# Performance work log

Hardware: AMD Instinct MI355X
Metric: run time of the kernel (lower is better)

Reference implementation:

```python
import math
import jax, jax.numpy as jnp
import numpy as np

NQ, NK = 16384, 4096
QDIM, KDIM, MID = 512, 256, 256


def setup_inputs() -> dict:
    key = jax.random.key(0)
    k1, k2, k3, k4, k5, k6, k7, k8 = jax.random.split(key, 8)
    return {
        "global_embeddings": jax.random.normal(k1, (NQ, QDIM), dtype=jnp.float32),
        "substruct_embeddings": jax.random.normal(k2, (NK, KDIM), dtype=jnp.float32),
        "substruct_weight": jax.random.uniform(k3, (NK,), dtype=jnp.float32),
        "mask": jax.random.randint(k4, (NQ, NK), 0, 2, dtype=jnp.int32),
        "Wq": jax.random.normal(k5, (MID, QDIM), dtype=jnp.float32) / math.sqrt(QDIM),
        "bq": jax.random.normal(k6, (MID,), dtype=jnp.float32) * 0.01,
        "Wk": jax.random.normal(k7, (MID, KDIM), dtype=jnp.float32) / math.sqrt(KDIM),
        "bk": jax.random.normal(k8, (MID,), dtype=jnp.float32) * 0.01,
    }


def reference(global_embeddings, substruct_embeddings, substruct_weight, mask, Wq, bq, Wk, bk):
    # Q/K projections (torch Linear: x @ W.T + b)
    Q = global_embeddings @ Wq.T + bq            # [NQ, MID]
    K = substruct_embeddings @ Wk.T + bk         # [NK, MID]
    scores = (Q @ K.T) / math.sqrt(MID)          # [NQ, NK]
    scores = jnp.where(mask == 0, -jnp.inf, scores)
    attn = jax.nn.softmax(scores, axis=-1)       # row-wise stable softmax
    # torch.diag(w) @ E  ==  elementwise row scaling
    V = substruct_weight[:, None] * substruct_embeddings  # [NK, KDIM]
    return attn @ V                              # [NQ, KDIM]
```

## Files before the change

kernel.cpp:

```cpp
#include <hip/hip_runtime.h>
#include <hip/hip_bf16.h>

typedef __bf16 bf16_t;
typedef bf16_t bf16x8 __attribute__((ext_vector_type(8)));
typedef float  f32x4  __attribute__((ext_vector_type(4)));
typedef unsigned long long u64;
typedef unsigned int u32;

#define MFMA16(A,B,C) __builtin_amdgcn_mfma_f32_16x16x32_bf16((A),(B),(C),0,0,0)


static __device__ __forceinline__ void gl_lds16(const bf16_t* g, void* l) {
    __builtin_amdgcn_global_load_lds(
        (const __attribute__((address_space(1))) u32*)(const void*)g,
        (__attribute__((address_space(3))) u32*)l, 16, 0, 0);
}

template<int KA, bool SWZ>
__global__ __launch_bounds__(256)
void proj_kernel(const float* __restrict__ A, const float* __restrict__ W,
                 const float* __restrict__ b, bf16_t* __restrict__ C,
                 float scale)
{
    __shared__ bf16_t Alds[64][40];
    __shared__ bf16_t Wlds[256][40];

    const int t  = threadIdx.x;
    const int w  = t >> 6, l = t & 63, lr = l & 15, lg = l >> 4;
    const int m0 = blockIdx.x * 64;

    f32x4 acc[16];
#pragma unroll
    for (int tt = 0; tt < 16; ++tt) acc[tt] = (f32x4){0.f, 0.f, 0.f, 0.f};

    const int ar  = t >> 2;
    const int ac8 = (t & 3) * 8;

    for (int kb = 0; kb < KA / 32; ++kb) {
        {
            const float* ap = A + (size_t)(m0 + ar) * KA + kb * 32 + ac8;
            float4 a0 = *(const float4*)ap;
            float4 a1 = *(const float4*)(ap + 4);
            bf16x8 av;
            av[0]=(bf16_t)a0.x; av[1]=(bf16_t)a0.y; av[2]=(bf16_t)a0.z; av[3]=(bf16_t)a0.w;
            av[4]=(bf16_t)a1.x; av[5]=(bf16_t)a1.y; av[6]=(bf16_t)a1.z; av[7]=(bf16_t)a1.w;
            *(bf16x8*)&Alds[ar][ac8] = av;
        }
#pragma unroll
        for (int c = 0; c < 4; ++c) {
            int e8 = c * 256 + t;
            int wr = e8 >> 2, wc8 = (e8 & 3) * 8;
            const float* wp = W + (size_t)wr * KA + kb * 32 + wc8;
            float4 w0 = *(const float4*)wp;
            float4 w1 = *(const float4*)(wp + 4);
            bf16x8 wv;
            wv[0]=(bf16_t)w0.x; wv[1]=(bf16_t)w0.y; wv[2]=(bf16_t)w0.z; wv[3]=(bf16_t)w0.w;
            wv[4]=(bf16_t)w1.x; wv[5]=(bf16_t)w1.y; wv[6]=(bf16_t)w1.z; wv[7]=(bf16_t)w1.w;
            *(bf16x8*)&Wlds[wr][wc8] = wv;
        }
        __syncthreads();

        bf16x8 af = *(bf16x8*)&Alds[w * 16 + lr][lg * 8];
#pragma unroll
        for (int tt = 0; tt < 16; ++tt) {
            bf16x8 bfrag = *(bf16x8*)&Wlds[tt * 16 + lr][lg * 8];
            acc[tt] = MFMA16(af, bfrag, acc[tt]);
        }
        __syncthreads();
    }

#pragma unroll
    for (int tt = 0; tt < 16; ++tt) {
        int col = tt * 16 + lr;
        float bias = b[col];
#pragma unroll
        for (int r = 0; r < 4; ++r) {
            int row = m0 + w * 16 + lg * 4 + r;
            int colS = col;
            if (SWZ) colS = (((col >> 3) ^ (row & 7)) << 3) | (col & 7);
            C[(size_t)row * 256 + colS] = (bf16_t)((acc[tt][r] + bias) * scale);
        }
    }
}

__global__ __launch_bounds__(256)
void buildvt_kernel(const float* __restrict__ S, const float* __restrict__ wgt,
                    bf16_t* __restrict__ VT)
{
    int i = blockIdx.x * 256 + threadIdx.x;
    int d = i >> 12, k = i & 4095;
    int kt = (k & ~63) | (((((k >> 3) & 7) ^ (d & 7)) << 3)) | (k & 7);
    VT[i] = (bf16_t)(wgt[kt] * S[(size_t)kt * 256 + d]);
}

template<bool SPLIT>
__global__ __launch_bounds__(256, 2)
void attn_kernel(const bf16_t* __restrict__ Qb, const bf16_t* __restrict__ Kb,
                 const bf16_t* __restrict__ VT, const int* __restrict__ mask,
                 float* __restrict__ out, float* __restrict__ pacc,
                 float* __restrict__ pm, float* __restrict__ pl)
{
    __shared__ __align__(16) char Kraw[32768];
    __shared__ __align__(16) char Vraw[32768];
    __shared__ __align__(16) char Praw[8192];

    const int t  = threadIdx.x;
    const int w  = t >> 6, l = t & 63, lr = l & 15, lg = l >> 4;
    const int q0 = blockIdx.x * 64;
    const int qw = q0 + w * 16;
    const int half = SPLIT ? (int)blockIdx.y : 0;
    const int NT   = SPLIT ? 32 : 64;
    const int kb0  = half * NT;

    bf16x8 qf[8];
    {
        const bf16_t* qrow = Qb + (size_t)(qw + lr) * 256;
#pragma unroll
        for (int kk = 0; kk < 8; ++kk)
            qf[kk] = *(const bf16x8*)(qrow + kk * 32 + lg * 8);
    }

    bf16x8 vone;
#pragma unroll
    for (int j = 0; j < 8; ++j) vone[j] = (bf16_t)1.0f;

    f32x4 acc[16];
#pragma unroll
    for (int dt = 0; dt < 16; ++dt) acc[dt] = (f32x4){0.f, 0.f, 0.f, 0.f};
    f32x4 lacc = (f32x4){0.f, 0.f, 0.f, 0.f};
    float mrow[4];
#pragma unroll
    for (int r = 0; r < 4; ++r) mrow[r] = -1e30f;

    for (int tb = 0; tb < NT; ++tb) {
        const int kb = kb0 + tb;

        int4 mv[4];
#pragma unroll
        for (int r = 0; r < 4; ++r)
            mv[r] = *(const int4*)(mask + (size_t)(qw + 4 * lg + r) * 4096
                                   + kb * 64 + lr * 4);

#pragma unroll
        for (int i = 0; i < 8; ++i) {
            int row = w * 16 + i * 2 + (l >> 5);
            gl_lds16(Kb + (size_t)(kb * 64 + row) * 256 + (l & 31) * 8,
                     Kraw + (w * 16 + i * 2) * 512);
        }
#pragma unroll
        for (int i = 0; i < 8; ++i) {
            int d = w * 64 + i * 8 + (l >> 3);
            gl_lds16(VT + (size_t)d * 4096 + kb * 64 + (l & 7) * 8,
                     Vraw + (w * 64 + i * 8) * 128);
        }

        u64 rowbits[4];
#pragma unroll
        for (int r = 0; r < 4; ++r) {
            u64 b0 = __ballot(mv[r].x != 0);
            u64 b1 = __ballot(mv[r].y != 0);
            u64 b2 = __ballot(mv[r].z != 0);
            u64 b3 = __ballot(mv[r].w != 0);
            u64 w01  = (lr & 1) ? b1 : b0;
            u64 w23  = (lr & 1) ? b3 : b2;
            u64 wsel = (lr & 2) ? w23 : w01;
            rowbits[r] = wsel >> (lg * 16 + (lr >> 2));
        }
        __syncthreads();

        f32x4 s[4];
#pragma unroll
        for (int tt = 0; tt < 4; ++tt) {
            f32x4 sv = (f32x4){0.f, 0.f, 0.f, 0.f};
#pragma unroll
            for (int kk = 0; kk < 8; ++kk) {
                bf16x8 kf = *(bf16x8*)(Kraw + (((tt * 16 + lr) * 512)
                                | ((((kk * 4 + lg) ^ (lr & 7)) << 4))));
                sv = MFMA16(qf[kk], kf, sv);
            }
            s[tt] = sv;
        }
#pragma unroll
        for (int tt = 0; tt < 4; ++tt)
#pragma unroll
            for (int r = 0; r < 4; ++r) {
                bool keep = ((rowbits[r] >> (4 * tt)) & 1ull) != 0;
                s[tt][r] = keep ? s[tt][r] : -1e30f;
            }

        float bm[4];
#pragma unroll
        for (int r = 0; r < 4; ++r)
            bm[r] = fmaxf(fmaxf(s[0][r], s[1][r]), fmaxf(s[2][r], s[3][r]));
#pragma unroll
        for (int off = 1; off < 16; off <<= 1)
#pragma unroll
            for (int r = 0; r < 4; ++r)
                bm[r] = fmaxf(bm[r], __shfl_xor(bm[r], off));

        bool need = false;
#pragma unroll
        for (int r = 0; r < 4; ++r) need = need || (bm[r] > mrow[r] + 8.f);
        if (__any(need)) {
#pragma unroll
            for (int r = 0; r < 4; ++r) {
                float mn = fmaxf(mrow[r], bm[r]);
                float fr = __expf(mrow[r] - mn);
                mrow[r] = mn;
                lacc[r] *= fr;
#pragma unroll
                for (int dt = 0; dt < 16; ++dt) acc[dt][r] *= fr;
            }
        }

#pragma unroll
        for (int tt = 0; tt < 4; ++tt)
#pragma unroll
            for (int r = 0; r < 4; ++r) {
                int prow = w * 16 + lg * 4 + r;
                *(bf16_t*)(Praw + ((prow * 128 + (tt * 16 + lr) * 2)
                                   ^ ((prow & 7) << 4)))
                    = (bf16_t)__expf(s[tt][r] - mrow[r]);
            }
        asm volatile("s_waitcnt lgkmcnt(0)" ::: "memory");
        __builtin_amdgcn_sched_barrier(0);

        bf16x8 pa0, pa1;
        {
            int prow = w * 16 + lr;
            pa0 = *(bf16x8*)(Praw + ((prow * 128 + (0 * 4 + lg) * 16)
                                     ^ ((prow & 7) << 4)));
            pa1 = *(bf16x8*)(Praw + ((prow * 128 + (1 * 4 + lg) * 16)
                                     ^ ((prow & 7) << 4)));
        }
        lacc = MFMA16(pa0, vone, lacc);
        lacc = MFMA16(pa1, vone, lacc);
#pragma unroll
        for (int dt = 0; dt < 16; ++dt) {
            int vrow = dt * 16 + lr;
            bf16x8 v0 = *(bf16x8*)(Vraw + ((vrow * 128)
                            | ((((0 * 4 + lg) ^ (lr & 7)) << 4))));
            bf16x8 v1 = *(bf16x8*)(Vraw + ((vrow * 128)
                            | ((((1 * 4 + lg) ^ (lr & 7)) << 4))));
            acc[dt] = MFMA16(pa0, v0, acc[dt]);
            acc[dt] = MFMA16(pa1, v1, acc[dt]);
        }
        __syncthreads();
    }

    if (SPLIT) {
        float* pa = pacc + (size_t)half * 16384 * 256;
#pragma unroll
        for (int r = 0; r < 4; ++r) {
            int row = qw + lg * 4 + r;
#pragma unroll
            for (int dt = 0; dt < 16; ++dt)
                pa[(size_t)row * 256 + dt * 16 + lr] = acc[dt][r];
            if (lr == 0) {
                pm[half * 16384 + row] = mrow[r];
                pl[half * 16384 + row] = lacc[r];
            }
        }
    } else {
#pragma unroll
        for (int r = 0; r < 4; ++r) {
            float inv = 1.0f / lacc[r];
#pragma unroll
            for (int dt = 0; dt < 16; ++dt)
                out[(size_t)(qw + lg * 4 + r) * 256 + dt * 16 + lr] = acc[dt][r] * inv;
        }
    }
}

__global__ __launch_bounds__(256)
void combine_kernel(const float* __restrict__ pacc, const float* __restrict__ pm,
                    const float* __restrict__ pl, float* __restrict__ out)
{
    int idx = blockIdx.x * 256 + threadIdx.x;
    int row = idx >> 6, c4 = (idx & 63) * 4;
    float m0 = pm[row], m1 = pm[16384 + row];
    float l0 = pl[row], l1 = pl[16384 + row];
    float m  = fmaxf(m0, m1);
    float a  = __expf(m0 - m), b = __expf(m1 - m);
    float inv = 1.0f / (l0 * a + l1 * b);
    float4 x0 = *(const float4*)(pacc + (size_t)row * 256 + c4);
    float4 x1 = *(const float4*)(pacc + (size_t)16384 * 256 + (size_t)row * 256 + c4);
    float4 o;
    o.x = (x0.x * a + x1.x * b) * inv;
    o.y = (x0.y * a + x1.y * b) * inv;
    o.z = (x0.z * a + x1.z * b) * inv;
    o.w = (x0.w * a + x1.w * b) * inv;
    *(float4*)(out + (size_t)row * 256 + c4) = o;
}

extern "C" void kernel_launch(void* const* d_in, const int* in_sizes, int n_in,
                              void* d_out, int out_size, void* d_ws, size_t ws_size,
                              hipStream_t stream)
{
    const float* gE   = (const float*)d_in[0];
    const float* sE   = (const float*)d_in[1];
    const float* wgt  = (const float*)d_in[2];
    const int*   mask = (const int*)  d_in[3];
    const float* Wq   = (const float*)d_in[4];
    const float* bq   = (const float*)d_in[5];
    const float* Wk   = (const float*)d_in[6];
    const float* bk   = (const float*)d_in[7];
    float* out = (float*)d_out;

    char* ws = (char*)d_ws;
    bf16_t* Qb = (bf16_t*)ws;
    bf16_t* Kb = (bf16_t*)(ws + 8388608);
    bf16_t* VT = (bf16_t*)(ws + 10485760);
    float*  pacc = (float*)(ws + 12582912);
    float*  pm   = (float*)(ws + 46137344);
    float*  pl   = (float*)(ws + 46268416);
    const size_t need_full = 46399488;
    const size_t need_min  = 12582912;

    if (ws_size < need_min) return;

    proj_kernel<512, false><<<dim3(256, 1), 256, 0, stream>>>(gE, Wq, bq, Qb, 0.0625f);
    proj_kernel<256, true ><<<dim3(64, 1), 256, 0, stream>>>(sE, Wk, bk, Kb, 1.0f);
    buildvt_kernel<<<4096, 256, 0, stream>>>(sE, wgt, VT);

    if (ws_size >= need_full) {
        attn_kernel<true><<<dim3(256, 2), 256, 0, stream>>>(
            Qb, Kb, VT, mask, out, pacc, pm, pl);
        combine_kernel<<<4096, 256, 0, stream>>>(pacc, pm, pl, out);
    } else {
        attn_kernel<false><<<dim3(256, 1), 256, 0, stream>>>(
            Qb, Kb, VT, mask, out, nullptr, nullptr, nullptr);
    }
}
```

Baseline: 210.5 us.

## Double-buffer K/V tiles in LDS and widen attention blocks to eight waves

The attention kernel now uses 512-thread blocks covering 128 query rows. Each K/V tile staged in LDS is therefore shared by twice as many rows, which halves staging traffic per row. K and V are double-buffered, so the next tile is prefetched while the current one is computed, and one barrier per iteration is dropped. LDS use rises to about 144KB per block, which allows only one block per CU. The launch bound of (512,2) also caps VGPRs per thread at about 128, which risks register spills given the large accumulator and Q-fragment state.

```diff
diff --git a/kernel.cpp b/kernel.cpp
--- a/kernel.cpp
+++ b/kernel.cpp
@@ -94,20 +94,19 @@
 }
 
 template<bool SPLIT>
-__global__ __launch_bounds__(256, 2)
+__global__ __launch_bounds__(512, 2)
 void attn_kernel(const bf16_t* __restrict__ Qb, const bf16_t* __restrict__ Kb,
                  const bf16_t* __restrict__ VT, const int* __restrict__ mask,
                  float* __restrict__ out, float* __restrict__ pacc,
                  float* __restrict__ pm, float* __restrict__ pl)
 {
-    __shared__ __align__(16) char Kraw[32768];
-    __shared__ __align__(16) char Vraw[32768];
-    __shared__ __align__(16) char Praw[8192];
+    __shared__ __align__(16) char Kraw[2][32768];
+    __shared__ __align__(16) char Vraw[2][32768];
+    __shared__ __align__(16) char Praw[16384];
 
     const int t  = threadIdx.x;
     const int w  = t >> 6, l = t & 63, lr = l & 15, lg = l >> 4;
-    const int q0 = blockIdx.x * 64;
-    const int qw = q0 + w * 16;
+    const int qw = blockIdx.x * 128 + w * 16;
     const int half = SPLIT ? (int)blockIdx.y : 0;
     const int NT   = SPLIT ? 32 : 64;
     const int kb0  = half * NT;
@@ -132,27 +131,30 @@
 #pragma unroll
     for (int r = 0; r < 4; ++r) mrow[r] = -1e30f;
 
-    for (int tb = 0; tb < NT; ++tb) {
-        const int kb = kb0 + tb;
-
+    auto stage = [&](int kb, char* kd, char* vd) {
+#pragma unroll
+        for (int i = 0; i < 4; ++i) {
+            int row = w * 8 + i * 2 + (l >> 5);
+            gl_lds16(Kb + (size_t)(kb * 64 + row) * 256 + (l & 31) * 8,
+                     kd + (w * 8 + i * 2) * 512);
+        }
+#pragma unroll
+        for (int i = 0; i < 4; ++i) {
+            int d = w * 32 + i * 8 + (l >> 3);
+            gl_lds16(VT + (size_t)d * 4096 + kb * 64 + (l & 7) * 8,
+                     vd + (w * 32 + i * 8) * 128);
+        }
+    };
+
+    auto iter = [&](int kb, char* kcur, char* vcur, char* knxt, char* vnxt,
+                    bool do_stage) {
         int4 mv[4];
 #pragma unroll
         for (int r = 0; r < 4; ++r)
             mv[r] = *(const int4*)(mask + (size_t)(qw + 4 * lg + r) * 4096
                                    + kb * 64 + lr * 4);
 
-#pragma unroll
-        for (int i = 0; i < 8; ++i) {
-            int row = w * 16 + i * 2 + (l >> 5);
-            gl_lds16(Kb + (size_t)(kb * 64 + row) * 256 + (l & 31) * 8,
-                     Kraw + (w * 16 + i * 2) * 512);
-        }
-#pragma unroll
-        for (int i = 0; i < 8; ++i) {
-            int d = w * 64 + i * 8 + (l >> 3);
-            gl_lds16(VT + (size_t)d * 4096 + kb * 64 + (l & 7) * 8,
-                     Vraw + (w * 64 + i * 8) * 128);
-        }
+        if (do_stage) stage(kb + 1, knxt, vnxt);
 
         u64 rowbits[4];
 #pragma unroll
@@ -166,7 +168,6 @@
             u64 wsel = (lr & 2) ? w23 : w01;
             rowbits[r] = wsel >> (lg * 16 + (lr >> 2));
         }
-        __syncthreads();
 
         f32x4 s[4];
 #pragma unroll
@@ -174,7 +175,7 @@
             f32x4 sv = (f32x4){0.f, 0.f, 0.f, 0.f};
 #pragma unroll
             for (int kk = 0; kk < 8; ++kk) {
-                bf16x8 kf = *(bf16x8*)(Kraw + (((tt * 16 + lr) * 512)
+                bf16x8 kf = *(bf16x8*)(kcur + (((tt * 16 + lr) * 512)
                                 | ((((kk * 4 + lg) ^ (lr & 7)) << 4))));
                 sv = MFMA16(qf[kk], kf, sv);
             }
@@ -238,14 +239,24 @@
 #pragma unroll
         for (int dt = 0; dt < 16; ++dt) {
             int vrow = dt * 16 + lr;
-            bf16x8 v0 = *(bf16x8*)(Vraw + ((vrow * 128)
+            bf16x8 v0 = *(bf16x8*)(vcur + ((vrow * 128)
                             | ((((0 * 4 + lg) ^ (lr & 7)) << 4))));
-            bf16x8 v1 = *(bf16x8*)(Vraw + ((vrow * 128)
+            bf16x8 v1 = *(bf16x8*)(vcur + ((vrow * 128)
                             | ((((1 * 4 + lg) ^ (lr & 7)) << 4))));
             acc[dt] = MFMA16(pa0, v0, acc[dt]);
             acc[dt] = MFMA16(pa1, v1, acc[dt]);
         }
         __syncthreads();
+    };
+
+    stage(kb0, &Kraw[0][0], &Vraw[0][0]);
+    __syncthreads();
+
+    for (int tb = 0; tb < NT; tb += 2) {
+        iter(kb0 + tb,     &Kraw[0][0], &Vraw[0][0], &Kraw[1][0], &Vraw[1][0],
+             true);
+        iter(kb0 + tb + 1, &Kraw[1][0], &Vraw[1][0], &Kraw[0][0], &Vraw[0][0],
+             tb + 2 < NT);
     }
 
     if (SPLIT) {
@@ -324,11 +335,11 @@
     buildvt_kernel<<<4096, 256, 0, stream>>>(sE, wgt, VT);
 
     if (ws_size >= need_full) {
-        attn_kernel<true><<<dim3(256, 2), 256, 0, stream>>>(
+        attn_kernel<true><<<dim3(128, 2), 512, 0, stream>>>(
             Qb, Kb, VT, mask, out, pacc, pm, pl);
         combine_kernel<<<4096, 256, 0, stream>>>(pacc, pm, pl, out);
     } else {
-        attn_kernel<false><<<dim3(256, 1), 256, 0, stream>>>(
+        attn_kernel<false><<<dim3(128, 1), 512, 0, stream>>>(
             Qb, Kb, VT, mask, out, nullptr, nullptr, nullptr);
     }
 }
```

After: 207.0 us. About the same (-1.7%).

## Halve key tile to 32, split keys four ways, raise attention occupancy

Applied to the files above, without the earlier changes.

The attention kernel now processes 32-key tiles instead of 64, which halves LDS use and lets launch bounds request four blocks per CU instead of two. The key range is split four ways instead of two, and the combine kernel merges four partial softmax states. The LDS XOR swizzles for V and P are dropped, so the VT build no longer permutes indices. The aim is more parallelism and latency hiding, at the cost of more partial-accumulator traffic, more synchronisation per key, possible LDS bank conflicts, and tighter register limits that may cause spills given the 64 accumulator floats per thread.

```diff
diff --git a/kernel.cpp b/kernel.cpp
--- a/kernel.cpp
+++ b/kernel.cpp
@@ -89,28 +89,26 @@
 {
     int i = blockIdx.x * 256 + threadIdx.x;
     int d = i >> 12, k = i & 4095;
-    int kt = (k & ~63) | (((((k >> 3) & 7) ^ (d & 7)) << 3)) | (k & 7);
-    VT[i] = (bf16_t)(wgt[kt] * S[(size_t)kt * 256 + d]);
-}
-
-template<bool SPLIT>
-__global__ __launch_bounds__(256, 2)
+    VT[i] = (bf16_t)(wgt[k] * S[(size_t)k * 256 + d]);
+}
+
+template<int SPLITN>
+__global__ __launch_bounds__(256, 4)
 void attn_kernel(const bf16_t* __restrict__ Qb, const bf16_t* __restrict__ Kb,
                  const bf16_t* __restrict__ VT, const int* __restrict__ mask,
                  float* __restrict__ out, float* __restrict__ pacc,
                  float* __restrict__ pm, float* __restrict__ pl)
 {
-    __shared__ __align__(16) char Kraw[32768];
-    __shared__ __align__(16) char Vraw[32768];
-    __shared__ __align__(16) char Praw[8192];
+    __shared__ __align__(16) char Kraw[16384];
+    __shared__ __align__(16) char Vraw[16384];
+    __shared__ __align__(16) char Praw[4096];
 
     const int t  = threadIdx.x;
     const int w  = t >> 6, l = t & 63, lr = l & 15, lg = l >> 4;
-    const int q0 = blockIdx.x * 64;
-    const int qw = q0 + w * 16;
-    const int half = SPLIT ? (int)blockIdx.y : 0;
-    const int NT   = SPLIT ? 32 : 64;
-    const int kb0  = half * NT;
+    const int qw = blockIdx.x * 64 + w * 16;
+    const int part = SPLITN > 1 ? (int)blockIdx.y : 0;
+    const int NT   = 128 / SPLITN;
+    const int kb0  = part * NT;
 
     bf16x8 qf[8];
     {
@@ -135,23 +133,23 @@
     for (int tb = 0; tb < NT; ++tb) {
         const int kb = kb0 + tb;
 
-        int4 mv[4];
+        int2 mv[4];
 #pragma unroll
         for (int r = 0; r < 4; ++r)
-            mv[r] = *(const int4*)(mask + (size_t)(qw + 4 * lg + r) * 4096
-                                   + kb * 64 + lr * 4);
-
-#pragma unroll
-        for (int i = 0; i < 8; ++i) {
-            int row = w * 16 + i * 2 + (l >> 5);
-            gl_lds16(Kb + (size_t)(kb * 64 + row) * 256 + (l & 31) * 8,
-                     Kraw + (w * 16 + i * 2) * 512);
-        }
-#pragma unroll
-        for (int i = 0; i < 8; ++i) {
-            int d = w * 64 + i * 8 + (l >> 3);
-            gl_lds16(VT + (size_t)d * 4096 + kb * 64 + (l & 7) * 8,
-                     Vraw + (w * 64 + i * 8) * 128);
+            mv[r] = *(const int2*)(mask + (size_t)(qw + 4 * lg + r) * 4096
+                                   + kb * 32 + lr * 2);
+
+#pragma unroll
+        for (int i = 0; i < 4; ++i) {
+            int row = w * 8 + i * 2 + (l >> 5);
+            gl_lds16(Kb + (size_t)(kb * 32 + row) * 256 + (l & 31) * 8,
+                     Kraw + (w * 8 + i * 2) * 512);
+        }
+#pragma unroll
+        for (int i = 0; i < 4; ++i) {
+            int d = w * 64 + i * 16 + (l >> 2);
+            gl_lds16(VT + (size_t)d * 4096 + kb * 32 + (l & 3) * 8,
+                     Vraw + (w * 64 + i * 16) * 64);
         }
 
         u64 rowbits[4];
@@ -159,18 +157,14 @@
         for (int r = 0; r < 4; ++r) {
             u64 b0 = __ballot(mv[r].x != 0);
             u64 b1 = __ballot(mv[r].y != 0);
-            u64 b2 = __ballot(mv[r].z != 0);
-            u64 b3 = __ballot(mv[r].w != 0);
-            u64 w01  = (lr & 1) ? b1 : b0;
-            u64 w23  = (lr & 1) ? b3 : b2;
-            u64 wsel = (lr & 2) ? w23 : w01;
-            rowbits[r] = wsel >> (lg * 16 + (lr >> 2));
+            u64 sel = (lr & 1) ? b1 : b0;
+            rowbits[r] = sel >> (lg * 16 + (lr >> 1));
         }
         __syncthreads();
 
-        f32x4 s[4];
-#pragma unroll
-        for (int tt = 0; tt < 4; ++tt) {
+        f32x4 s[2];
+#pragma unroll
+        for (int tt = 0; tt < 2; ++tt) {
             f32x4 sv = (f32x4){0.f, 0.f, 0.f, 0.f};
 #pragma unroll
             for (int kk = 0; kk < 8; ++kk) {
@@ -181,17 +175,17 @@
             s[tt] = sv;
         }
 #pragma unroll
-        for (int tt = 0; tt < 4; ++tt)
+        for (int tt = 0; tt < 2; ++tt)
 #pragma unroll
             for (int r = 0; r < 4; ++r) {
-                bool keep = ((rowbits[r] >> (4 * tt)) & 1ull) != 0;
+                bool keep = ((rowbits[r] >> (8 * tt)) & 1ull) != 0;
                 s[tt][r] = keep ? s[tt][r] : -1e30f;
             }
 
         float bm[4];
 #pragma unroll
         for (int r = 0; r < 4; ++r)
-            bm[r] = fmaxf(fmaxf(s[0][r], s[1][r]), fmaxf(s[2][r], s[3][r]));
+            bm[r] = fmaxf(s[0][r], s[1][r]);
 #pragma unroll
         for (int off = 1; off < 16; off <<= 1)
 #pragma unroll
@@ -214,42 +208,28 @@
         }
 
 #pragma unroll
-        for (int tt = 0; tt < 4; ++tt)
+        for (int tt = 0; tt < 2; ++tt)
 #pragma unroll
             for (int r = 0; r < 4; ++r) {
                 int prow = w * 16 + lg * 4 + r;
-                *(bf16_t*)(Praw + ((prow * 128 + (tt * 16 + lr) * 2)
-                                   ^ ((prow & 7) << 4)))
+                *(bf16_t*)(Praw + prow * 64 + (tt * 16 + lr) * 2)
                     = (bf16_t)__expf(s[tt][r] - mrow[r]);
             }
         asm volatile("s_waitcnt lgkmcnt(0)" ::: "memory");
         __builtin_amdgcn_sched_barrier(0);
 
-        bf16x8 pa0, pa1;
-        {
-            int prow = w * 16 + lr;
-            pa0 = *(bf16x8*)(Praw + ((prow * 128 + (0 * 4 + lg) * 16)
-                                     ^ ((prow & 7) << 4)));
-            pa1 = *(bf16x8*)(Praw + ((prow * 128 + (1 * 4 + lg) * 16)
-                                     ^ ((prow & 7) << 4)));
-        }
+        bf16x8 pa0 = *(bf16x8*)(Praw + (w * 16 + lr) * 64 + lg * 16);
         lacc = MFMA16(pa0, vone, lacc);
-        lacc = MFMA16(pa1, vone, lacc);
 #pragma unroll
         for (int dt = 0; dt < 16; ++dt) {
-            int vrow = dt * 16 + lr;
-            bf16x8 v0 = *(bf16x8*)(Vraw + ((vrow * 128)
-                            | ((((0 * 4 + lg) ^ (lr & 7)) << 4))));
-            bf16x8 v1 = *(bf16x8*)(Vraw + ((vrow * 128)
-                            | ((((1 * 4 + lg) ^ (lr & 7)) << 4))));
-            acc[dt] = MFMA16(pa0, v0, acc[dt]);
-            acc[dt] = MFMA16(pa1, v1, acc[dt]);
+            bf16x8 vf = *(bf16x8*)(Vraw + (dt * 16 + lr) * 64 + lg * 16);
+            acc[dt] = MFMA16(pa0, vf, acc[dt]);
         }
         __syncthreads();
     }
 
-    if (SPLIT) {
-        float* pa = pacc + (size_t)half * 16384 * 256;
+    if (SPLITN > 1) {
+        float* pa = pacc + (size_t)part * 16384 * 256;
 #pragma unroll
         for (int r = 0; r < 4; ++r) {
             int row = qw + lg * 4 + r;
@@ -257,8 +237,8 @@
             for (int dt = 0; dt < 16; ++dt)
                 pa[(size_t)row * 256 + dt * 16 + lr] = acc[dt][r];
             if (lr == 0) {
-                pm[half * 16384 + row] = mrow[r];
-                pl[half * 16384 + row] = lacc[r];
+                pm[part * 16384 + row] = mrow[r];
+                pl[part * 16384 + row] = lacc[r];
             }
         }
     } else {
@@ -278,18 +258,25 @@
 {
     int idx = blockIdx.x * 256 + threadIdx.x;
     int row = idx >> 6, c4 = (idx & 63) * 4;
-    float m0 = pm[row], m1 = pm[16384 + row];
-    float l0 = pl[row], l1 = pl[16384 + row];
-    float m  = fmaxf(m0, m1);
-    float a  = __expf(m0 - m), b = __expf(m1 - m);
-    float inv = 1.0f / (l0 * a + l1 * b);
-    float4 x0 = *(const float4*)(pacc + (size_t)row * 256 + c4);
-    float4 x1 = *(const float4*)(pacc + (size_t)16384 * 256 + (size_t)row * 256 + c4);
-    float4 o;
-    o.x = (x0.x * a + x1.x * b) * inv;
-    o.y = (x0.y * a + x1.y * b) * inv;
-    o.z = (x0.z * a + x1.z * b) * inv;
-    o.w = (x0.w * a + x1.w * b) * inv;
+    float m = -1e30f;
+#pragma unroll
+    for (int s = 0; s < 4; ++s) m = fmaxf(m, pm[s * 16384 + row]);
+    float f[4], den = 0.f;
+#pragma unroll
+    for (int s = 0; s < 4; ++s) {
+        f[s] = __expf(pm[s * 16384 + row] - m);
+        den += pl[s * 16384 + row] * f[s];
+    }
+    float inv = 1.0f / den;
+    float4 o = {0.f, 0.f, 0.f, 0.f};
+#pragma unroll
+    for (int s = 0; s < 4; ++s) {
+        float4 x = *(const float4*)(pacc + (size_t)s * 16384 * 256
+                                    + (size_t)row * 256 + c4);
+        o.x += x.x * f[s]; o.y += x.y * f[s];
+        o.z += x.z * f[s]; o.w += x.w * f[s];
+    }
+    o.x *= inv; o.y *= inv; o.z *= inv; o.w *= inv;
     *(float4*)(out + (size_t)row * 256 + c4) = o;
 }
 
@@ -312,9 +299,9 @@
     bf16_t* Kb = (bf16_t*)(ws + 8388608);
     bf16_t* VT = (bf16_t*)(ws + 10485760);
     float*  pacc = (float*)(ws + 12582912);
-    float*  pm   = (float*)(ws + 46137344);
-    float*  pl   = (float*)(ws + 46268416);
-    const size_t need_full = 46399488;
+    float*  pm   = (float*)(ws + 79691776);
+    float*  pl   = (float*)(ws + 79953920);
+    const size_t need_full = 80216064;
     const size_t need_min  = 12582912;
 
     if (ws_size < need_min) return;
@@ -324,11 +311,11 @@
     buildvt_kernel<<<4096, 256, 0, stream>>>(sE, wgt, VT);
 
     if (ws_size >= need_full) {
-        attn_kernel<true><<<dim3(256, 2), 256, 0, stream>>>(
+        attn_kernel<4><<<dim3(256, 4), 256, 0, stream>>>(
             Qb, Kb, VT, mask, out, pacc, pm, pl);
         combine_kernel<<<4096, 256, 0, stream>>>(pacc, pm, pl, out);
     } else {
-        attn_kernel<false><<<dim3(256, 1), 256, 0, stream>>>(
+        attn_kernel<1><<<dim3(256, 1), 256, 0, stream>>>(
             Qb, Kb, VT, mask, out, nullptr, nullptr, nullptr);
     }
 }
```

Result: slower. 507.3 us (+141.0%).
